# Performance work log

Hardware: AMD Instinct MI355X
Metric: run time of the kernel (lower is better)

## Reference

```python
import jax, jax.numpy as jnp
import numpy as np

NEG_INF = -9e15
ALPHA = 0.2  # LeakyReLU negative slope

N = 8192
D_IN = 512
D_OUT = 256


def setup_inputs() -> dict:
    key = jax.random.key(0)
    k1, k2, k3, k4, k5 = jax.random.split(key, 5)
    features = jax.random.normal(k1, (N, D_IN), dtype=jnp.float32)
    adjacency_matrix = jax.random.randint(k2, (N, N), 0, 2, dtype=jnp.int32)
    # learned params (torch Linear stores [out, in]; we use [in, out] layout)
    s_phi = 1.0 / np.sqrt(D_IN)
    W_phi = jax.random.uniform(k3, (D_IN, D_OUT), jnp.float32, -s_phi, s_phi)
    s_v = 1.0 / np.sqrt(D_OUT)
    w_mu = jax.random.uniform(k4, (D_OUT,), jnp.float32, -s_v, s_v)
    w_xi = jax.random.uniform(k5, (D_OUT,), jnp.float32, -s_v, s_v)
    return {"features": features, "adjacency_matrix": adjacency_matrix,
            "W_phi": W_phi, "w_mu": w_mu, "w_xi": w_xi}


def reference(features, adjacency_matrix, W_phi, w_mu, w_xi):
    h = features @ W_phi                                   # [N, d_out]
    mu = h @ w_mu                                          # [N]
    xi = h @ w_xi                                          # [N]
    e = mu[:, None] + xi[None, :]                          # [N, N] additive scores
    e = jnp.where(e >= 0, e, ALPHA * e)                    # LeakyReLU
    e = jnp.where(adjacency_matrix > 0, e, NEG_INF)        # mask non-edges
    a = jax.nn.softmax(e, axis=1)                          # row softmax (dropout p=0)
    out = a @ h                                            # weighted aggregation
    return jax.nn.elu(out)
```

## Files before the change

### kernel.cpp

```cpp
#include <hip/hip_runtime.h>
#include <cstdint>
#include <cstddef>


#define LOG2E 1.44269504f

typedef __attribute__((ext_vector_type(8))) short short8;
typedef __attribute__((ext_vector_type(4))) float floatx4;

using uint_as1 = __attribute__((address_space(1))) unsigned int;
using uint_as3 = __attribute__((address_space(3))) unsigned int;

__device__ __forceinline__ void gld_lds16(const void* g, void* l) {
  __builtin_amdgcn_global_load_lds((const uint_as1*)g, (uint_as3*)l, 16, 0, 0);
}

__device__ __forceinline__ unsigned short f2b(float f) {
  unsigned u = __float_as_uint(f);
  u += 0x7fffu + ((u >> 16) & 1u);
  return (unsigned short)(u >> 16);
}
__device__ __forceinline__ float b2f(short s) {
  return __uint_as_float(((unsigned)(unsigned short)s) << 16);
}

__device__ __forceinline__ unsigned cvtpk_bf16(float a, float b) {
  unsigned r;
  asm("v_cvt_pk_bf16_f32 %0, %1, %2" : "=v"(r) : "v"(a), "v"(b));
  return r;
}

__global__ void k_cvt_features(const float* __restrict__ f, unsigned short* __restrict__ fb) {
  int tid = blockIdx.x * 256 + threadIdx.x;
  float4 v = ((const float4*)f)[tid];
  ushort4 o = {f2b(v.x), f2b(v.y), f2b(v.z), f2b(v.w)};
  *(ushort4*)&fb[tid * 4] = o;
}

__global__ void k_prep_wt(const float* __restrict__ w, unsigned short* __restrict__ wt) {
  int tid = blockIdx.x * 256 + threadIdx.x;
  int n = tid >> 9, k = tid & 511;
  wt[n * 512 + k] = f2b(w[k * 256 + n]);
}

__global__ void k_prep_p(const float* __restrict__ w, const float* __restrict__ wmu,
                         const float* __restrict__ wxi, float* __restrict__ pmu,
                         float* __restrict__ pxi) {
  int tid = blockIdx.x * 256 + threadIdx.x;
  int k = tid >> 2, seg = tid & 3;
  float sm = 0.f, sx = 0.f;
  int base = k * 256 + seg * 64;
#pragma unroll
  for (int c = 0; c < 64; c += 4) {
    float4 wv = *(const float4*)&w[base + c];
    float4 mv = *(const float4*)&wmu[seg * 64 + c];
    float4 xv = *(const float4*)&wxi[seg * 64 + c];
    sm += wv.x * mv.x + wv.y * mv.y + wv.z * mv.z + wv.w * mv.w;
    sx += wv.x * xv.x + wv.y * xv.y + wv.z * xv.z + wv.w * xv.w;
  }
  sm += __shfl_xor(sm, 1); sm += __shfl_xor(sm, 2);
  sx += __shfl_xor(sx, 1); sx += __shfl_xor(sx, 2);
  if (seg == 0) { pmu[k] = sm; pxi[k] = sx; }
}

__global__ void k_mu_xi(const unsigned short* __restrict__ fb, const float* __restrict__ pmu,
                        const float* __restrict__ pxi, float* __restrict__ Emu,
                        float* __restrict__ Fmu, float* __restrict__ Exi,
                        float* __restrict__ Fxi) {
  int w = threadIdx.x >> 6, l = threadIdx.x & 63;
  int i = blockIdx.x * 4 + w;
  short8 fv = *(const short8*)&fb[i * 512 + l * 8];
  float m = 0.f, x = 0.f;
#pragma unroll
  for (int c = 0; c < 8; ++c) {
    float fvf = b2f(fv[c]);
    m = fmaf(fvf, pmu[l * 8 + c], m);
    x = fmaf(fvf, pxi[l * 8 + c], x);
  }
#pragma unroll
  for (int off = 32; off > 0; off >>= 1) {
    m += __shfl_xor(m, off);
    x += __shfl_xor(x, off);
  }
  if (l == 0) {
    float ms = m * LOG2E, xs = x * LOG2E;
    Emu[i] = __builtin_amdgcn_exp2f(ms);
    Fmu[i] = __builtin_amdgcn_exp2f(0.2f * ms);
    Exi[i] = __builtin_amdgcn_exp2f(xs);
    Fxi[i] = __builtin_amdgcn_exp2f(0.2f * xs);
  }
}

__global__ __launch_bounds__(256, 2) void k_gemm1(const unsigned short* __restrict__ fb,
                                                  const unsigned short* __restrict__ wt,
                                                  unsigned short* __restrict__ ht) {
  __shared__ __align__(16) unsigned short As[64 * 64];
  __shared__ __align__(16) unsigned short Bs[128 * 64];
  int t = threadIdx.x, w = t >> 6, l = t & 63;
  int bm_ = blockIdx.x >> 1, bn = blockIdx.x & 1;
  int m0 = bm_ * 64, n0 = bn * 128;
  int lr = l >> 3, lg = l & 7, g = lg ^ lr;
  int kg = l >> 4, ln = l & 15;
  floatx4 zero = {0.f, 0.f, 0.f, 0.f};
  floatx4 acc[4][2];
#pragma unroll
  for (int mf = 0; mf < 4; ++mf)
#pragma unroll
    for (int nf = 0; nf < 2; ++nf) acc[mf][nf] = zero;

  for (int it = 0; it < 8; ++it) {
    int k0 = it * 64;
#pragma unroll
    for (int q = 0; q < 2; ++q) {
      int row = w * 16 + q * 8 + lr;
      const void* gp = fb + (size_t)(m0 + row) * 512 + k0 + g * 8;
      int lb = __builtin_amdgcn_readfirstlane((w * 16 + q * 8) * 64);
      gld_lds16(gp, &As[lb]);
    }
#pragma unroll
    for (int q = 0; q < 4; ++q) {
      int row = w * 32 + q * 8 + lr;
      const void* gp = wt + (size_t)(n0 + row) * 512 + k0 + g * 8;
      int lb = __builtin_amdgcn_readfirstlane((w * 32 + q * 8) * 64);
      gld_lds16(gp, &Bs[lb]);
    }
    __syncthreads();
#pragma unroll
    for (int ks = 0; ks < 2; ++ks) {
      int gg = ks * 4 + kg;
      int swz = (gg ^ (ln & 7)) * 8;
      short8 bfr[2];
#pragma unroll
      for (int nf = 0; nf < 2; ++nf)
        bfr[nf] = *(const short8*)&Bs[(w * 32 + nf * 16 + ln) * 64 + swz];
#pragma unroll
      for (int mf = 0; mf < 4; ++mf) {
        short8 afr = *(const short8*)&As[(mf * 16 + ln) * 64 + swz];
#pragma unroll
        for (int nf = 0; nf < 2; ++nf)
          acc[mf][nf] = __builtin_amdgcn_mfma_f32_16x16x32_bf16(afr, bfr[nf], acc[mf][nf], 0, 0, 0);
      }
    }
    __syncthreads();
  }
#pragma unroll
  for (int mf = 0; mf < 4; ++mf)
#pragma unroll
    for (int nf = 0; nf < 2; ++nf) {
      int ng = n0 + w * 32 + nf * 16 + ln;
      int mg = m0 + mf * 16 + kg * 4;
      ushort4 o = {f2b(acc[mf][nf][0]), f2b(acc[mf][nf][1]),
                   f2b(acc[mf][nf][2]), f2b(acc[mf][nf][3])};
      *(ushort4*)&ht[(size_t)ng * 8192 + mg] = o;
    }
}

__global__ __launch_bounds__(512, 1) void k_gatt13(const int* __restrict__ adjm,
                                                   const unsigned short* __restrict__ ht,
                                                   const float* __restrict__ Emu,
                                                   const float* __restrict__ Fmu,
                                                   const float* __restrict__ Exi,
                                                   const float* __restrict__ Fxi,
                                                   float* __restrict__ nump,
                                                   float* __restrict__ zpart) {
  __shared__ __align__(16) unsigned short Bs[4][256 * 32];
  __shared__ __align__(16) float EfE[1024];
  __shared__ __align__(16) float EfF[1024];

  int t = threadIdx.x, w = t >> 6, l = t & 63;
  int ln = l & 15, kg = l >> 4;
  int jb = blockIdx.x & 7, ig = blockIdx.x >> 3;
  int i0 = ig * 256;
  int jc0 = jb * 1024;

  if (t < 256) {
    *(float4*)&EfE[t * 4] = *(const float4*)&Exi[jc0 + t * 4];
  } else {
    int t2 = t - 256;
    *(float4*)&EfF[t2 * 4] = *(const float4*)&Fxi[jc0 + t2 * 4];
  }

  float EM[2], FM[2];
#pragma unroll
  for (int mf = 0; mf < 2; ++mf) {
    int i = i0 + w * 32 + mf * 16 + ln;
    EM[mf] = Emu[i];
    FM[mf] = Fmu[i];
  }

  const int* ar0 = adjm + (size_t)(i0 + w * 32 + ln) * 8192 + jc0 + kg * 8;
  const int* ar1 = ar0 + (size_t)16 * 8192;

  floatx4 zero = {0.f, 0.f, 0.f, 0.f};
  floatx4 acc[2][16];
#pragma unroll
  for (int mf = 0; mf < 2; ++mf)
#pragma unroll
    for (int nf = 0; nf < 16; ++nf) acc[mf][nf] = zero;
  float zacc[2] = {0.f, 0.f};

#define STAGE_B(win_, b_)                                                   \
  {                                                                         \
    int j0_ = jc0 + (win_) * 32;                                            \
    _Pragma("unroll")                                                       \
    for (int q = 0; q < 2; ++q) {                                           \
      int rowbase = w * 32 + q * 16;                                        \
      int row = rowbase + (l >> 2);                                         \
      int g = (l & 3) ^ ((row >> 1) & 3);                                   \
      const void* gp = ht + (size_t)row * 8192 + j0_ + g * 8;               \
      int lb = __builtin_amdgcn_readfirstlane((b_) * (256 * 32) + rowbase * 32); \
      gld_lds16(gp, &((unsigned short*)Bs)[lb]);                            \
    }                                                                       \
  }

  STAGE_B(0, 0);
  STAGE_B(1, 1);
  __syncthreads();

  for (int win = 0; win < 32; ++win) {
    int bR = win & 3;
    if (win < 31) {
      asm volatile("s_waitcnt vmcnt(2)" ::: "memory");
    } else {
      asm volatile("s_waitcnt vmcnt(0)" ::: "memory");
    }
    __builtin_amdgcn_s_barrier();
    asm volatile("" ::: "memory");

    int joff = win * 32;
    int4 a0 = *(const int4*)(ar0 + joff);
    int4 a1 = *(const int4*)(ar0 + joff + 4);
    int4 a2 = *(const int4*)(ar1 + joff);
    int4 a3 = *(const int4*)(ar1 + joff + 4);

    int jl = win * 32 + kg * 8;
    float4 e0 = *(const float4*)&EfE[jl];
    float4 e1 = *(const float4*)&EfE[jl + 4];
    float4 f0 = *(const float4*)&EfF[jl];
    float4 f1 = *(const float4*)&EfF[jl + 4];

    short8 af[2];
#pragma unroll
    for (int mf = 0; mf < 2; ++mf) {
      int av[8];
      if (mf == 0) {
        av[0] = a0.x; av[1] = a0.y; av[2] = a0.z; av[3] = a0.w;
        av[4] = a1.x; av[5] = a1.y; av[6] = a1.z; av[7] = a1.w;
      } else {
        av[0] = a2.x; av[1] = a2.y; av[2] = a2.z; av[3] = a2.w;
        av[4] = a3.x; av[5] = a3.y; av[6] = a3.z; av[7] = a3.w;
      }
      float ex[8] = {e0.x, e0.y, e0.z, e0.w, e1.x, e1.y, e1.z, e1.w};
      float fx[8] = {f0.x, f0.y, f0.z, f0.w, f1.x, f1.y, f1.z, f1.w};
      float A = EM[mf], F = FM[mf];
      union { unsigned u[4]; short8 s; } cv;
      float zs = 0.f;
#pragma unroll
      for (int p = 0; p < 4; ++p) {
        float m0 = fmaxf(A * ex[2 * p], F * fx[2 * p]);
        float m1 = fmaxf(A * ex[2 * p + 1], F * fx[2 * p + 1]);
        m0 = (av[2 * p] != 0) ? m0 : 0.f;
        m1 = (av[2 * p + 1] != 0) ? m1 : 0.f;
        zs += m0;
        zs += m1;
        cv.u[p] = cvtpk_bf16(m0, m1);
      }
      zacc[mf] += zs;
      af[mf] = cv.s;
    }
#pragma unroll
    for (int qtr = 0; qtr < 4; ++qtr) {
      short8 bfv[4];
#pragma unroll
      for (int nf = 0; nf < 4; ++nf) {
        int n = qtr * 64 + nf * 16 + ln;
        bfv[nf] = *(const short8*)&Bs[bR][n * 32 + ((kg ^ ((n >> 1) & 3)) * 8)];
      }
#pragma unroll
      for (int mf = 0; mf < 2; ++mf)
#pragma unroll
        for (int nf = 0; nf < 4; ++nf)
          acc[mf][qtr * 4 + nf] = __builtin_amdgcn_mfma_f32_16x16x32_bf16(
              af[mf], bfv[nf], acc[mf][qtr * 4 + nf], 0, 0, 0);
    }
    if (win < 30) {
      STAGE_B(win + 2, (win + 2) & 3);
    }
  }
#undef STAGE_B

#pragma unroll
  for (int mf = 0; mf < 2; ++mf) {
    float z = zacc[mf];
    z += __shfl_xor(z, 16);
    z += __shfl_xor(z, 32);
    if (l < 16) zpart[(size_t)jb * 8192 + i0 + w * 32 + mf * 16 + ln] = z;
  }

  float* np = nump + (size_t)jb * (8192 * 256);
#pragma unroll
  for (int mf = 0; mf < 2; ++mf) {
    int rowb = i0 + w * 32 + mf * 16 + kg * 4;
#pragma unroll
    for (int r = 0; r < 4; ++r) {
      float* rp = np + (size_t)(rowb + r) * 256;
#pragma unroll
      for (int nf = 0; nf < 16; ++nf)
        rp[nf * 16 + ln] = acc[mf][nf][r];
    }
  }
}

__global__ void k_final(const float* __restrict__ nump, const float* __restrict__ zpart,
                        float* __restrict__ out) {
  int tid = blockIdx.x * 256 + threadIdx.x;
  int i = tid >> 6;
  float z = 0.f;
#pragma unroll
  for (int p = 0; p < 8; ++p) z += zpart[(size_t)p * 8192 + i];
  float zi = 1.0f / z;
  float4 v = {0.f, 0.f, 0.f, 0.f};
#pragma unroll
  for (int p = 0; p < 8; ++p) {
    float4 s = *(const float4*)&nump[(size_t)p * (8192 * 256) + tid * 4];
    v.x += s.x; v.y += s.y; v.z += s.z; v.w += s.w;
  }
  v.x *= zi; v.y *= zi; v.z *= zi; v.w *= zi;
  v.x = (v.x > 0.f) ? v.x : (__builtin_amdgcn_exp2f(v.x * LOG2E) - 1.f);
  v.y = (v.y > 0.f) ? v.y : (__builtin_amdgcn_exp2f(v.y * LOG2E) - 1.f);
  v.z = (v.z > 0.f) ? v.z : (__builtin_amdgcn_exp2f(v.z * LOG2E) - 1.f);
  v.w = (v.w > 0.f) ? v.w : (__builtin_amdgcn_exp2f(v.w * LOG2E) - 1.f);
  *(float4*)&out[tid * 4] = v;
}

extern "C" void kernel_launch(void* const* d_in, const int* in_sizes, int n_in,
                              void* d_out, int out_size, void* d_ws, size_t ws_size,
                              hipStream_t stream) {
  const float* features = (const float*)d_in[0];
  const int* adjm = (const int*)d_in[1];
  const float* W_phi = (const float*)d_in[2];
  const float* w_mu = (const float*)d_in[3];
  const float* w_xi = (const float*)d_in[4];
  float* out = (float*)d_out;

  char* ws = (char*)d_ws;
  unsigned short* fb  = (unsigned short*)(ws + 0);
  unsigned short* ht  = (unsigned short*)(ws + 8388608);
  unsigned short* wt  = (unsigned short*)(ws + 12582912);
  float* pmu = (float*)(ws + 12845056);
  float* pxi = (float*)(ws + 12847104);
  float* Emu = (float*)(ws + 12849152);
  float* Fmu = (float*)(ws + 12881920);
  float* Exi = (float*)(ws + 12914688);
  float* Fxi = (float*)(ws + 12947456);
  float* zpart = (float*)(ws + 12980224);
  float* nump = (float*)(ws + 25165824);

  k_cvt_features<<<4096, 256, 0, stream>>>(features, fb);
  k_prep_wt<<<512, 256, 0, stream>>>(W_phi, wt);
  k_prep_p<<<8, 256, 0, stream>>>(W_phi, w_mu, w_xi, pmu, pxi);
  k_mu_xi<<<2048, 256, 0, stream>>>(fb, pmu, pxi, Emu, Fmu, Exi, Fxi);
  k_gemm1<<<256, 256, 0, stream>>>(fb, wt, ht);
  k_gatt13<<<256, 512, 0, stream>>>(adjm, ht, Emu, Fmu, Exi, Fxi, nump, zpart);
  k_final<<<2048, 256, 0, stream>>>(nump, zpart, out);
}
```

Baseline: 452.1 us.

## Shrink attention blocks to 64 rows with 256 threads for multi-block occupancy

Each attention block now covers 64 rows instead of 256, using 4 waves of 16 rows each, and the grid grows from 256 to 1024 blocks with launch bounds targeting 3 blocks per CU. The four-deep asynchronous LDS ring with hand-placed waitcnt and barrier is replaced by a simpler double buffer and a __syncthreads each window. The aim is to fill more CUs and hide latency through occupancy rather than explicit pipelining. The cost is that each B tile staged in LDS is reused by only 64 rows, so ht is read from global memory four times as often.

Measured after the change: 465.1 us. 1.03x slower.

```diff
diff --git a/kernel.cpp b/kernel.cpp
--- a/kernel.cpp
+++ b/kernel.cpp
@@ -155,7 +155,7 @@
     }
 }
 
-__global__ __launch_bounds__(512, 1) void k_gatt13(const int* __restrict__ adjm,
+__global__ __launch_bounds__(256, 3) void k_gatt14(const int* __restrict__ adjm,
                                                    const unsigned short* __restrict__ ht,
                                                    const float* __restrict__ Emu,
                                                    const float* __restrict__ Fmu,
@@ -163,48 +163,38 @@
                                                    const float* __restrict__ Fxi,
                                                    float* __restrict__ nump,
                                                    float* __restrict__ zpart) {
-  __shared__ __align__(16) unsigned short Bs[4][256 * 32];
+  __shared__ __align__(16) unsigned short Bs[2][256 * 32];
   __shared__ __align__(16) float EfE[1024];
   __shared__ __align__(16) float EfF[1024];
 
   int t = threadIdx.x, w = t >> 6, l = t & 63;
   int ln = l & 15, kg = l >> 4;
   int jb = blockIdx.x & 7, ig = blockIdx.x >> 3;
-  int i0 = ig * 256;
+  int i0 = ig * 64;
   int jc0 = jb * 1024;
 
-  if (t < 256) {
-    *(float4*)&EfE[t * 4] = *(const float4*)&Exi[jc0 + t * 4];
-  } else {
-    int t2 = t - 256;
-    *(float4*)&EfF[t2 * 4] = *(const float4*)&Fxi[jc0 + t2 * 4];
-  }
-
-  float EM[2], FM[2];
-#pragma unroll
-  for (int mf = 0; mf < 2; ++mf) {
-    int i = i0 + w * 32 + mf * 16 + ln;
-    EM[mf] = Emu[i];
-    FM[mf] = Fmu[i];
-  }
-
-  const int* ar0 = adjm + (size_t)(i0 + w * 32 + ln) * 8192 + jc0 + kg * 8;
-  const int* ar1 = ar0 + (size_t)16 * 8192;
+  *(float4*)&EfE[t * 4] = *(const float4*)&Exi[jc0 + t * 4];
+  {
+    *(float4*)&EfF[t * 4] = *(const float4*)&Fxi[jc0 + t * 4];
+  }
+
+  float EM = Emu[i0 + w * 16 + ln];
+  float FM = Fmu[i0 + w * 16 + ln];
+
+  const int* ar0 = adjm + (size_t)(i0 + w * 16 + ln) * 8192 + jc0 + kg * 8;
 
   floatx4 zero = {0.f, 0.f, 0.f, 0.f};
-  floatx4 acc[2][16];
-#pragma unroll
-  for (int mf = 0; mf < 2; ++mf)
-#pragma unroll
-    for (int nf = 0; nf < 16; ++nf) acc[mf][nf] = zero;
-  float zacc[2] = {0.f, 0.f};
+  floatx4 acc[16];
+#pragma unroll
+  for (int nf = 0; nf < 16; ++nf) acc[nf] = zero;
+  float zacc = 0.f;
 
 #define STAGE_B(win_, b_)                                                   \
   {                                                                         \
     int j0_ = jc0 + (win_) * 32;                                            \
     _Pragma("unroll")                                                       \
-    for (int q = 0; q < 2; ++q) {                                           \
-      int rowbase = w * 32 + q * 16;                                        \
+    for (int q = 0; q < 4; ++q) {                                           \
+      int rowbase = w * 64 + q * 16;                                        \
       int row = rowbase + (l >> 2);                                         \
       int g = (l & 3) ^ ((row >> 1) & 3);                                   \
       const void* gp = ht + (size_t)row * 8192 + j0_ + g * 8;               \
@@ -214,24 +204,16 @@
   }
 
   STAGE_B(0, 0);
-  STAGE_B(1, 1);
   __syncthreads();
 
   for (int win = 0; win < 32; ++win) {
-    int bR = win & 3;
+    int buf = win & 1;
     if (win < 31) {
-      asm volatile("s_waitcnt vmcnt(2)" ::: "memory");
-    } else {
-      asm volatile("s_waitcnt vmcnt(0)" ::: "memory");
-    }
-    __builtin_amdgcn_s_barrier();
-    asm volatile("" ::: "memory");
-
+      STAGE_B(win + 1, buf ^ 1);
+    }
     int joff = win * 32;
     int4 a0 = *(const int4*)(ar0 + joff);
     int4 a1 = *(const int4*)(ar0 + joff + 4);
-    int4 a2 = *(const int4*)(ar1 + joff);
-    int4 a3 = *(const int4*)(ar1 + joff + 4);
 
     int jl = win * 32 + kg * 8;
     float4 e0 = *(const float4*)&EfE[jl];
@@ -239,34 +221,25 @@
     float4 f0 = *(const float4*)&EfF[jl];
     float4 f1 = *(const float4*)&EfF[jl + 4];
 
-    short8 af[2];
-#pragma unroll
-    for (int mf = 0; mf < 2; ++mf) {
-      int av[8];
-      if (mf == 0) {
-        av[0] = a0.x; av[1] = a0.y; av[2] = a0.z; av[3] = a0.w;
-        av[4] = a1.x; av[5] = a1.y; av[6] = a1.z; av[7] = a1.w;
-      } else {
-        av[0] = a2.x; av[1] = a2.y; av[2] = a2.z; av[3] = a2.w;
-        av[4] = a3.x; av[5] = a3.y; av[6] = a3.z; av[7] = a3.w;
-      }
+    short8 af;
+    {
+      int av[8] = {a0.x, a0.y, a0.z, a0.w, a1.x, a1.y, a1.z, a1.w};
       float ex[8] = {e0.x, e0.y, e0.z, e0.w, e1.x, e1.y, e1.z, e1.w};
       float fx[8] = {f0.x, f0.y, f0.z, f0.w, f1.x, f1.y, f1.z, f1.w};
-      float A = EM[mf], F = FM[mf];
       union { unsigned u[4]; short8 s; } cv;
       float zs = 0.f;
 #pragma unroll
       for (int p = 0; p < 4; ++p) {
-        float m0 = fmaxf(A * ex[2 * p], F * fx[2 * p]);
-        float m1 = fmaxf(A * ex[2 * p + 1], F * fx[2 * p + 1]);
+        float m0 = fmaxf(EM * ex[2 * p], FM * fx[2 * p]);
+        float m1 = fmaxf(EM * ex[2 * p + 1], FM * fx[2 * p + 1]);
         m0 = (av[2 * p] != 0) ? m0 : 0.f;
         m1 = (av[2 * p + 1] != 0) ? m1 : 0.f;
         zs += m0;
         zs += m1;
         cv.u[p] = cvtpk_bf16(m0, m1);
       }
-      zacc[mf] += zs;
-      af[mf] = cv.s;
+      zacc += zs;
+      af = cv.s;
     }
 #pragma unroll
     for (int qtr = 0; qtr < 4; ++qtr) {
@@ -274,39 +247,33 @@
 #pragma unroll
       for (int nf = 0; nf < 4; ++nf) {
         int n = qtr * 64 + nf * 16 + ln;
-        bfv[nf] = *(const short8*)&Bs[bR][n * 32 + ((kg ^ ((n >> 1) & 3)) * 8)];
+        bfv[nf] = *(const short8*)&Bs[buf][n * 32 + ((kg ^ ((n >> 1) & 3)) * 8)];
       }
 #pragma unroll
-      for (int mf = 0; mf < 2; ++mf)
-#pragma unroll
-        for (int nf = 0; nf < 4; ++nf)
-          acc[mf][qtr * 4 + nf] = __builtin_amdgcn_mfma_f32_16x16x32_bf16(
-              af[mf], bfv[nf], acc[mf][qtr * 4 + nf], 0, 0, 0);
-    }
-    if (win < 30) {
-      STAGE_B(win + 2, (win + 2) & 3);
-    }
+      for (int nf = 0; nf < 4; ++nf)
+        acc[qtr * 4 + nf] = __builtin_amdgcn_mfma_f32_16x16x32_bf16(
+            af, bfv[nf], acc[qtr * 4 + nf], 0, 0, 0);
+    }
+    __syncthreads();
   }
 #undef STAGE_B
 
-#pragma unroll
-  for (int mf = 0; mf < 2; ++mf) {
-    float z = zacc[mf];
+  {
+    float z = zacc;
     z += __shfl_xor(z, 16);
     z += __shfl_xor(z, 32);
-    if (l < 16) zpart[(size_t)jb * 8192 + i0 + w * 32 + mf * 16 + ln] = z;
+    if (l < 16) zpart[(size_t)jb * 8192 + i0 + w * 16 + ln] = z;
   }
 
   float* np = nump + (size_t)jb * (8192 * 256);
-#pragma unroll
-  for (int mf = 0; mf < 2; ++mf) {
-    int rowb = i0 + w * 32 + mf * 16 + kg * 4;
+  {
+    int rowb = i0 + w * 16 + kg * 4;
 #pragma unroll
     for (int r = 0; r < 4; ++r) {
       float* rp = np + (size_t)(rowb + r) * 256;
 #pragma unroll
       for (int nf = 0; nf < 16; ++nf)
-        rp[nf * 16 + ln] = acc[mf][nf][r];
+        rp[nf * 16 + ln] = acc[nf][r];
     }
   }
 }
@@ -361,6 +328,6 @@
   k_prep_p<<<8, 256, 0, stream>>>(W_phi, w_mu, w_xi, pmu, pxi);
   k_mu_xi<<<2048, 256, 0, stream>>>(fb, pmu, pxi, Emu, Fmu, Exi, Fxi);
   k_gemm1<<<256, 256, 0, stream>>>(fb, wt, ht);
-  k_gatt13<<<256, 512, 0, stream>>>(adjm, ht, Emu, Fmu, Exi, Fxi, nump, zpart);
+  k_gatt14<<<1024, 256, 0, stream>>>(adjm, ht, Emu, Fmu, Exi, Fxi, nump, zpart);
   k_final<<<2048, 256, 0, stream>>>(nump, zpart, out);
 }
```

## Fuse feature conversion and mu/xi projections into GEMM epilogue

Applied to the files above, without the earlier changes.

Removes the separate feature-to-bf16 conversion, weight projection and mu/xi kernels. The GEMM now loads fp32 features directly, converts them to bf16 in registers before writing to LDS, and reduces the accumulator tile against w_mu/w_xi in its epilogue to produce per-column-block partial mu/xi. The attention kernel sums the two partials and computes the exponentials itself. This saves three launches and a full bf16 feature round trip, but the A operand no longer uses async global-to-LDS loads, and mu/xi are now computed from bf16-rounded inputs with fp32 accumulation.

New measurement: 447.7 us. About the same (-1.0%).

```diff
diff --git a/kernel.cpp b/kernel.cpp
--- a/kernel.cpp
+++ b/kernel.cpp
@@ -20,9 +20,6 @@
   u += 0x7fffu + ((u >> 16) & 1u);
   return (unsigned short)(u >> 16);
 }
-__device__ __forceinline__ float b2f(short s) {
-  return __uint_as_float(((unsigned)(unsigned short)s) << 16);
-}
 
 __device__ __forceinline__ unsigned cvtpk_bf16(float a, float b) {
   unsigned r;
@@ -30,72 +27,23 @@
   return r;
 }
 
-__global__ void k_cvt_features(const float* __restrict__ f, unsigned short* __restrict__ fb) {
-  int tid = blockIdx.x * 256 + threadIdx.x;
-  float4 v = ((const float4*)f)[tid];
-  ushort4 o = {f2b(v.x), f2b(v.y), f2b(v.z), f2b(v.w)};
-  *(ushort4*)&fb[tid * 4] = o;
-}
-
 __global__ void k_prep_wt(const float* __restrict__ w, unsigned short* __restrict__ wt) {
   int tid = blockIdx.x * 256 + threadIdx.x;
   int n = tid >> 9, k = tid & 511;
   wt[n * 512 + k] = f2b(w[k * 256 + n]);
 }
 
-__global__ void k_prep_p(const float* __restrict__ w, const float* __restrict__ wmu,
-                         const float* __restrict__ wxi, float* __restrict__ pmu,
-                         float* __restrict__ pxi) {
-  int tid = blockIdx.x * 256 + threadIdx.x;
-  int k = tid >> 2, seg = tid & 3;
-  float sm = 0.f, sx = 0.f;
-  int base = k * 256 + seg * 64;
-#pragma unroll
-  for (int c = 0; c < 64; c += 4) {
-    float4 wv = *(const float4*)&w[base + c];
-    float4 mv = *(const float4*)&wmu[seg * 64 + c];
-    float4 xv = *(const float4*)&wxi[seg * 64 + c];
-    sm += wv.x * mv.x + wv.y * mv.y + wv.z * mv.z + wv.w * mv.w;
-    sx += wv.x * xv.x + wv.y * xv.y + wv.z * xv.z + wv.w * xv.w;
-  }
-  sm += __shfl_xor(sm, 1); sm += __shfl_xor(sm, 2);
-  sx += __shfl_xor(sx, 1); sx += __shfl_xor(sx, 2);
-  if (seg == 0) { pmu[k] = sm; pxi[k] = sx; }
-}
-
-__global__ void k_mu_xi(const unsigned short* __restrict__ fb, const float* __restrict__ pmu,
-                        const float* __restrict__ pxi, float* __restrict__ Emu,
-                        float* __restrict__ Fmu, float* __restrict__ Exi,
-                        float* __restrict__ Fxi) {
-  int w = threadIdx.x >> 6, l = threadIdx.x & 63;
-  int i = blockIdx.x * 4 + w;
-  short8 fv = *(const short8*)&fb[i * 512 + l * 8];
-  float m = 0.f, x = 0.f;
-#pragma unroll
-  for (int c = 0; c < 8; ++c) {
-    float fvf = b2f(fv[c]);
-    m = fmaf(fvf, pmu[l * 8 + c], m);
-    x = fmaf(fvf, pxi[l * 8 + c], x);
-  }
-#pragma unroll
-  for (int off = 32; off > 0; off >>= 1) {
-    m += __shfl_xor(m, off);
-    x += __shfl_xor(x, off);
-  }
-  if (l == 0) {
-    float ms = m * LOG2E, xs = x * LOG2E;
-    Emu[i] = __builtin_amdgcn_exp2f(ms);
-    Fmu[i] = __builtin_amdgcn_exp2f(0.2f * ms);
-    Exi[i] = __builtin_amdgcn_exp2f(xs);
-    Fxi[i] = __builtin_amdgcn_exp2f(0.2f * xs);
-  }
-}
-
-__global__ __launch_bounds__(256, 2) void k_gemm1(const unsigned short* __restrict__ fb,
-                                                  const unsigned short* __restrict__ wt,
-                                                  unsigned short* __restrict__ ht) {
+__global__ __launch_bounds__(256, 2) void k_gemm1m(const float* __restrict__ f,
+                                                   const unsigned short* __restrict__ wt,
+                                                   const float* __restrict__ wmu,
+                                                   const float* __restrict__ wxi,
+                                                   unsigned short* __restrict__ ht,
+                                                   float* __restrict__ mupart,
+                                                   float* __restrict__ xipart) {
   __shared__ __align__(16) unsigned short As[64 * 64];
   __shared__ __align__(16) unsigned short Bs[128 * 64];
+  __shared__ float musum[4][64];
+  __shared__ float xisum[4][64];
   int t = threadIdx.x, w = t >> 6, l = t & 63;
   int bm_ = blockIdx.x >> 1, bn = blockIdx.x & 1;
   int m0 = bm_ * 64, n0 = bn * 128;
@@ -113,9 +61,12 @@
 #pragma unroll
     for (int q = 0; q < 2; ++q) {
       int row = w * 16 + q * 8 + lr;
-      const void* gp = fb + (size_t)(m0 + row) * 512 + k0 + g * 8;
-      int lb = __builtin_amdgcn_readfirstlane((w * 16 + q * 8) * 64);
-      gld_lds16(gp, &As[lb]);
+      const float* fp = f + (size_t)(m0 + row) * 512 + k0 + g * 8;
+      float4 v0 = *(const float4*)fp;
+      float4 v1 = *(const float4*)(fp + 4);
+      uint4 d = {cvtpk_bf16(v0.x, v0.y), cvtpk_bf16(v0.z, v0.w),
+                 cvtpk_bf16(v1.x, v1.y), cvtpk_bf16(v1.z, v1.w)};
+      *(uint4*)&As[row * 64 + lg * 8] = d;
     }
 #pragma unroll
     for (int q = 0; q < 4; ++q) {
@@ -153,14 +104,38 @@
                    f2b(acc[mf][nf][2]), f2b(acc[mf][nf][3])};
       *(ushort4*)&ht[(size_t)ng * 8192 + mg] = o;
     }
-}
-
-__global__ __launch_bounds__(512, 1) void k_gatt13(const int* __restrict__ adjm,
+  float wma = wmu[n0 + w * 32 + ln], wmb = wmu[n0 + w * 32 + 16 + ln];
+  float wxa = wxi[n0 + w * 32 + ln], wxb = wxi[n0 + w * 32 + 16 + ln];
+#pragma unroll
+  for (int mf = 0; mf < 4; ++mf)
+#pragma unroll
+    for (int r = 0; r < 4; ++r) {
+      float ms = acc[mf][0][r] * wma + acc[mf][1][r] * wmb;
+      float xs = acc[mf][0][r] * wxa + acc[mf][1][r] * wxb;
+      ms += __shfl_xor(ms, 1); ms += __shfl_xor(ms, 2);
+      ms += __shfl_xor(ms, 4); ms += __shfl_xor(ms, 8);
+      xs += __shfl_xor(xs, 1); xs += __shfl_xor(xs, 2);
+      xs += __shfl_xor(xs, 4); xs += __shfl_xor(xs, 8);
+      if (ln == 0) {
+        musum[w][mf * 16 + kg * 4 + r] = ms;
+        xisum[w][mf * 16 + kg * 4 + r] = xs;
+      }
+    }
+  __syncthreads();
+  if (t < 64) {
+    float m_ = musum[0][t] + musum[1][t] + musum[2][t] + musum[3][t];
+    mupart[(size_t)bn * 8192 + m0 + t] = m_;
+  } else if (t < 128) {
+    int r = t - 64;
+    float x_ = xisum[0][r] + xisum[1][r] + xisum[2][r] + xisum[3][r];
+    xipart[(size_t)bn * 8192 + m0 + r] = x_;
+  }
+}
+
+__global__ __launch_bounds__(512, 1) void k_gatt16(const int* __restrict__ adjm,
                                                    const unsigned short* __restrict__ ht,
-                                                   const float* __restrict__ Emu,
-                                                   const float* __restrict__ Fmu,
-                                                   const float* __restrict__ Exi,
-                                                   const float* __restrict__ Fxi,
+                                                   const float* __restrict__ mupart,
+                                                   const float* __restrict__ xipart,
                                                    float* __restrict__ nump,
                                                    float* __restrict__ zpart) {
   __shared__ __align__(16) unsigned short Bs[4][256 * 32];
@@ -173,19 +148,32 @@
   int i0 = ig * 256;
   int jc0 = jb * 1024;
 
-  if (t < 256) {
-    *(float4*)&EfE[t * 4] = *(const float4*)&Exi[jc0 + t * 4];
-  } else {
-    int t2 = t - 256;
-    *(float4*)&EfF[t2 * 4] = *(const float4*)&Fxi[jc0 + t2 * 4];
+  {
+    int t2 = t & 255;
+    float4 xa = *(const float4*)&xipart[jc0 + t2 * 4];
+    float4 xb = *(const float4*)&xipart[8192 + jc0 + t2 * 4];
+    float x0 = (xa.x + xb.x) * LOG2E, x1 = (xa.y + xb.y) * LOG2E;
+    float x2 = (xa.z + xb.z) * LOG2E, x3 = (xa.w + xb.w) * LOG2E;
+    if (t < 256) {
+      EfE[t2 * 4 + 0] = __builtin_amdgcn_exp2f(x0);
+      EfE[t2 * 4 + 1] = __builtin_amdgcn_exp2f(x1);
+      EfE[t2 * 4 + 2] = __builtin_amdgcn_exp2f(x2);
+      EfE[t2 * 4 + 3] = __builtin_amdgcn_exp2f(x3);
+    } else {
+      EfF[t2 * 4 + 0] = __builtin_amdgcn_exp2f(0.2f * x0);
+      EfF[t2 * 4 + 1] = __builtin_amdgcn_exp2f(0.2f * x1);
+      EfF[t2 * 4 + 2] = __builtin_amdgcn_exp2f(0.2f * x2);
+      EfF[t2 * 4 + 3] = __builtin_amdgcn_exp2f(0.2f * x3);
+    }
   }
 
   float EM[2], FM[2];
 #pragma unroll
   for (int mf = 0; mf < 2; ++mf) {
     int i = i0 + w * 32 + mf * 16 + ln;
-    EM[mf] = Emu[i];
-    FM[mf] = Fmu[i];
+    float mu = (mupart[i] + mupart[8192 + i]) * LOG2E;
+    EM[mf] = __builtin_amdgcn_exp2f(mu);
+    FM[mf] = __builtin_amdgcn_exp2f(0.2f * mu);
   }
 
   const int* ar0 = adjm + (size_t)(i0 + w * 32 + ln) * 8192 + jc0 + kg * 8;
@@ -344,23 +332,15 @@
   float* out = (float*)d_out;
 
   char* ws = (char*)d_ws;
-  unsigned short* fb  = (unsigned short*)(ws + 0);
-  unsigned short* ht  = (unsigned short*)(ws + 8388608);
-  unsigned short* wt  = (unsigned short*)(ws + 12582912);
-  float* pmu = (float*)(ws + 12845056);
-  float* pxi = (float*)(ws + 12847104);
-  float* Emu = (float*)(ws + 12849152);
-  float* Fmu = (float*)(ws + 12881920);
-  float* Exi = (float*)(ws + 12914688);
-  float* Fxi = (float*)(ws + 12947456);
-  float* zpart = (float*)(ws + 12980224);
-  float* nump = (float*)(ws + 25165824);
-
-  k_cvt_features<<<4096, 256, 0, stream>>>(features, fb);
+  unsigned short* ht  = (unsigned short*)(ws + 0);
+  unsigned short* wt  = (unsigned short*)(ws + 4194304);
+  float* mupart = (float*)(ws + 4456448);
+  float* xipart = (float*)(ws + 4521984);
+  float* zpart  = (float*)(ws + 4587520);
+  float* nump   = (float*)(ws + 8388608);
+
   k_prep_wt<<<512, 256, 0, stream>>>(W_phi, wt);
-  k_prep_p<<<8, 256, 0, stream>>>(W_phi, w_mu, w_xi, pmu, pxi);
-  k_mu_xi<<<2048, 256, 0, stream>>>(fb, pmu, pxi, Emu, Fmu, Exi, Fxi);
-  k_gemm1<<<256, 256, 0, stream>>>(fb, wt, ht);
-  k_gatt13<<<256, 512, 0, stream>>>(adjm, ht, Emu, Fmu, Exi, Fxi, nump, zpart);
+  k_gemm1m<<<256, 256, 0, stream>>>(features, wt, w_mu, w_xi, ht, mupart, xipart);
+  k_gatt16<<<256, 512, 0, stream>>>(adjm, ht, mupart, xipart, nump, zpart);
   k_final<<<2048, 256, 0, stream>>>(nump, zpart, out);
 }
```
